# Performance work log

Measured on AMD Instinct MI355X. Metric: run time of the kernel, lower is better.

Reference implementation:

```python
import jax, jax.numpy as jnp
import numpy as np

B, T, S0 = 8, 4, 4096
D_MODEL, H, D, R, RANK = 2048, 16, 128, 64, 512
C = D - R  # content dim = 64


def _rope(x, positions):
    # x: [B, H, T, R]; rotate-half style RoPE as in the torch module
    half = x.shape[-1] // 2
    inv_freq = 1.0 / (10000.0 ** (jnp.arange(half, dtype=jnp.float32) / half))
    freqs = positions.astype(jnp.float32)[:, None] * inv_freq[None, :]  # [T, half]
    cos = jnp.cos(freqs)[None, None].astype(x.dtype)
    sin = jnp.sin(freqs)[None, None].astype(x.dtype)
    x1, x2 = x[..., :half], x[..., half:]
    return jnp.concatenate([x1 * cos - x2 * sin, x1 * sin + x2 * cos], axis=-1)


def setup_inputs() -> dict:
    key = jax.random.key(0)
    ks = jax.random.split(key, 9)
    s = 0.02
    return {
        "x": jax.random.normal(ks[0], (B, T, D_MODEL), jnp.float32),
        "cache_c_kv": jax.random.normal(ks[1], (B, S0, RANK), jnp.float32),
        "cache_k_rope": jax.random.normal(ks[2], (B, S0, H, R), jnp.float32),
        "w_q": jax.random.normal(ks[3], (D_MODEL, H * C), jnp.float32) * s,
        "w_q_rope": jax.random.normal(ks[4], (D_MODEL, H * R), jnp.float32) * s,
        "w_kv_down": jax.random.normal(ks[5], (D_MODEL, RANK), jnp.float32) * s,
        "w_kv_up": jax.random.normal(ks[6], (RANK, H * D), jnp.float32) * s,
        "w_k_rope": jax.random.normal(ks[7], (D_MODEL, H * R), jnp.float32) * s,
        "w_out": jax.random.normal(ks[8], (H * D, D_MODEL), jnp.float32) * s,
    }


def reference(x, cache_c_kv, cache_k_rope, w_q, w_q_rope, w_kv_down, w_kv_up, w_k_rope, w_out):
    cache_len = cache_c_kv.shape[1]
    positions = jnp.arange(cache_len, cache_len + T)

    # queries
    q_content = (x @ w_q).reshape(B, T, H, C).transpose(0, 2, 1, 3)        # [B,H,T,C]
    q_rope = (x @ w_q_rope).reshape(B, T, H, R).transpose(0, 2, 1, 3)      # [B,H,T,R]
    q_rope = _rope(q_rope, positions)
    q = jnp.concatenate([q_content, q_rope], axis=-1)                       # [B,H,T,D]

    # new compressed kv + rope keys, append to cache
    c_kv_new = x @ w_kv_down                                                # [B,T,RANK]
    k_rope_new = (x @ w_k_rope).reshape(B, T, H, R).transpose(0, 2, 1, 3)
    k_rope_new = _rope(k_rope_new, positions).transpose(0, 2, 1, 3)         # [B,T,H,R]
    c_kv = jnp.concatenate([cache_c_kv, c_kv_new], axis=1)                  # [B,S,RANK]
    k_rope = jnp.concatenate([cache_k_rope, k_rope_new], axis=1)            # [B,S,H,R]

    # decompress full cache every step (the expensive MLA pattern)
    S = c_kv.shape[1]
    kv = (c_kv @ w_kv_up).reshape(B, S, H, D)                               # [B,S,H,D]
    k_content = kv[..., :C].transpose(0, 2, 1, 3)                           # [B,H,S,C]
    v = kv.transpose(0, 2, 1, 3)                                            # [B,H,S,D]
    k = jnp.concatenate([k_content, k_rope.transpose(0, 2, 1, 3)], axis=-1) # [B,H,S,D]

    # kv_cache present => is_prefill False => no causal mask (faithful to source)
    scale = 1.0 / jnp.sqrt(jnp.asarray(D, dtype=q.dtype))
    scores = jnp.einsum('bhtd,bhsd->bhts', q, k) * scale
    attn = jax.nn.softmax(scores, axis=-1)
    out = jnp.einsum('bhts,bhsd->bhtd', attn, v)                            # [B,H,T,D]
    out = out.transpose(0, 2, 1, 3).reshape(B, T, H * D)
    return out @ w_out                                                       # [B,T,D_MODEL]
```

## Files before the change

kernel.cpp:

```cpp
#include <hip/hip_runtime.h>
#include <hip/hip_fp16.h>
#include <cmath>

#define BB 8
#define TT 4
#define HH 16
#define DDIM 128
#define RRDIM 64
#define CCDIM 64
#define RANKC 512
#define DMODEL 2048
#define S0C 4096
#define NQ 64
#define HD 2048
#define NACT 3584
#define NSC 65
#define NG 17
#define SPAD 4160
#define SCALE_ATT 0.08838834764831845f

typedef __attribute__((ext_vector_type(8))) short bf16x8;
typedef __attribute__((ext_vector_type(4))) float f32x4;
typedef unsigned short ushortT;

#define AIDX(row, kk) ((row)*132 + (((row)>>2)<<2) + (kk))

static __device__ __forceinline__ unsigned short f2bf(float x) {
  unsigned u = __float_as_uint(x);
  u += 0x7FFFu + ((u >> 16) & 1u);
  return (unsigned short)(u >> 16);
}
static __device__ __forceinline__ unsigned pk2(float a, float b) {
  return (unsigned)f2bf(a) | ((unsigned)f2bf(b) << 16);
}

__global__ __launch_bounds__(256) void k_front(const float* __restrict__ A,
                                               const float* __restrict__ w0,
                                               const float* __restrict__ w1,
                                               const float* __restrict__ w2,
                                               const float* __restrict__ w3,
                                               const float* __restrict__ cckv,
                                               float* __restrict__ part,
                                               ushortT* __restrict__ ckvB,
                                               ushortT* __restrict__ ckvT,
                                               float* __restrict__ rctab) {
  __shared__ float shf[4352];
  const int tid = threadIdx.x;
  const int bx = blockIdx.x;
  if (bx < 448) {
    const int cb = bx % 28;
    const int k0 = (bx / 28) * 128;
    const float* W; int N, lc0, off;
    if (cb < 8)       { W = w0; N = 1024; lc0 = cb * 128;        off = 0; }
    else if (cb < 16) { W = w1; N = 1024; lc0 = (cb - 8) * 128;  off = 1024; }
    else if (cb < 20) { W = w2; N = 512;  lc0 = (cb - 16) * 128; off = 2048; }
    else              { W = w3; N = 1024; lc0 = (cb - 20) * 128; off = 2560; }
    {
      const int row = tid >> 3;
      const int kseg = (tid & 7) * 16;
      const float4* s4 = reinterpret_cast<const float4*>(A + (size_t)row * DMODEL + k0 + kseg);
      float4 v0 = s4[0], v1 = s4[1], v2 = s4[2], v3 = s4[3];
      *reinterpret_cast<float4*>(&shf[AIDX(row, kseg)])      = v0;
      *reinterpret_cast<float4*>(&shf[AIDX(row, kseg + 4)])  = v1;
      *reinterpret_cast<float4*>(&shf[AIDX(row, kseg + 8)])  = v2;
      *reinterpret_cast<float4*>(&shf[AIDX(row, kseg + 12)]) = v3;
    }
    __syncthreads();
    const int cg = tid & 31;
    const int rg = tid >> 5;
    float acc[4][4];
    #pragma unroll
    for (int r = 0; r < 4; ++r)
      #pragma unroll
      for (int c = 0; c < 4; ++c) acc[r][c] = 0.f;
    #pragma unroll 4
    for (int kk = 0; kk < 128; ++kk) {
      const float4 w4 = *reinterpret_cast<const float4*>(W + (size_t)(k0 + kk) * N + lc0 + cg * 4);
      const float wv[4] = {w4.x, w4.y, w4.z, w4.w};
      #pragma unroll
      for (int r = 0; r < 4; ++r) {
        const float av = shf[AIDX(rg * 4 + r, kk)];
        #pragma unroll
        for (int c = 0; c < 4; ++c) acc[r][c] = fmaf(av, wv[c], acc[r][c]);
      }
    }
    #pragma unroll
    for (int r = 0; r < 4; ++r) {
      float4 o = make_float4(acc[r][0], acc[r][1], acc[r][2], acc[r][3]);
      *reinterpret_cast<float4*>(part + ((size_t)(bx / 28) * 32 + rg * 4 + r) * NACT + off + lc0 + cg * 4) = o;
    }
  } else if (bx < 960) {
    ushortT* tlds = reinterpret_cast<ushortT*>(shf);
    const int idx = bx - 448;
    const int b = idx >> 6, c = idx & 63;
    const float* src = cckv + ((size_t)b * S0C + c * 64) * RANKC;
    ushortT* dstB = ckvB + ((size_t)(b * NSC + c) * 64) * RANKC;
    ushortT* dstT = ckvT + ((size_t)(b * NSC + c) * RANKC) * 64;
    const int s = tid >> 2, rq = tid & 3;
    const int rloc = tid >> 1, shalf = (tid & 1) * 32;
    for (int slab = 0; slab < 4; ++slab) {
      const int r0 = slab * 128;
      unsigned pk_arr[16];
      #pragma unroll
      for (int i = 0; i < 8; ++i) {
        const float4 v = *reinterpret_cast<const float4*>(src + (size_t)s * RANKC + r0 + rq * 32 + i * 4);
        pk_arr[2 * i]     = pk2(v.x, v.y);
        pk_arr[2 * i + 1] = pk2(v.z, v.w);
        *reinterpret_cast<uint2*>(&tlds[s * 136 + rq * 32 + i * 4]) =
            make_uint2(pk_arr[2 * i], pk_arr[2 * i + 1]);
      }
      {
        uint4* db = reinterpret_cast<uint4*>(dstB + (size_t)s * RANKC + r0 + rq * 32);
        db[0] = make_uint4(pk_arr[0], pk_arr[1], pk_arr[2], pk_arr[3]);
        db[1] = make_uint4(pk_arr[4], pk_arr[5], pk_arr[6], pk_arr[7]);
        db[2] = make_uint4(pk_arr[8], pk_arr[9], pk_arr[10], pk_arr[11]);
        db[3] = make_uint4(pk_arr[12], pk_arr[13], pk_arr[14], pk_arr[15]);
      }
      __syncthreads();
      unsigned pkv[16];
      #pragma unroll
      for (int k = 0; k < 16; ++k) {
        const unsigned t0 = tlds[(shalf + 2 * k)     * 136 + rloc];
        const unsigned t1 = tlds[(shalf + 2 * k + 1) * 136 + rloc];
        pkv[k] = t0 | (t1 << 16);
      }
      uint4* d = reinterpret_cast<uint4*>(dstT + ((size_t)(r0 + rloc)) * 64 + shalf);
      d[0] = make_uint4(pkv[0], pkv[1], pkv[2], pkv[3]);
      d[1] = make_uint4(pkv[4], pkv[5], pkv[6], pkv[7]);
      d[2] = make_uint4(pkv[8], pkv[9], pkv[10], pkv[11]);
      d[3] = make_uint4(pkv[12], pkv[13], pkv[14], pkv[15]);
      __syncthreads();
    }
  } else {
    const int b = bx - 960;
    const uint4 z = make_uint4(0, 0, 0, 0);
    uint4* p = reinterpret_cast<uint4*>(ckvT + ((size_t)(b * NSC + 64) * RANKC) * 64);
    for (int i = tid; i < 4096; i += 256) p[i] = z;
    uint4* q = reinterpret_cast<uint4*>(ckvB + (((size_t)(b * NSC + 64) * 64) + 4) * RANKC);
    for (int i = tid; i < 3840; i += 256) q[i] = z;
    if (bx == 960 && tid < 128) {
      const int t = tid >> 5, j = tid & 31;
      const double fr = (double)(S0C + t) * pow(10000.0, -(double)j / 32.0);
      rctab[t * 32 + j]       = (float)cos(fr);
      rctab[128 + t * 32 + j] = (float)sin(fr);
    }
  }
}

__global__ __launch_bounds__(256) void k_mid(const float* __restrict__ part0,
                                             const float* __restrict__ cache_kr,
                                             const float* __restrict__ wup,
                                             const float* __restrict__ rctab,
                                             ushortT* __restrict__ qlat,
                                             ushortT* __restrict__ ckvB,
                                             ushortT* __restrict__ ckvT,
                                             __half* __restrict__ rs) {
  __shared__ float smid[2176];
  const int tid = threadIdx.x;
  const int bx = blockIdx.x;
  if (bx < 1152) {
    const int bh = bx / 9, sy = bx % 9;
    const int b = bh >> 4, h = bh & 15;
    float* raw_q = smid;
    float* raw_k = smid + 256;
    float* qr_l  = smid + 512;
    float* kr_l  = smid + 768;
    {
      const int t = tid >> 6, j = tid & 63;
      const size_t rowoff = (size_t)(b * TT + t) * NACT;
      float sq = 0.f, sk = 0.f;
      #pragma unroll 4
      for (int ks = 0; ks < 16; ++ks) {
        const float* pp = part0 + (size_t)ks * (32 * NACT) + rowoff;
        sq += pp[1024 + h * 64 + j];
        sk += pp[2560 + h * 64 + j];
      }
      raw_q[t * 64 + j] = sq;
      raw_k[t * 64 + j] = sk;
    }
    __syncthreads();
    {
      const int t = tid >> 6, j = tid & 63;
      const int j2 = j & 31;
      const float cs = rctab[t * 32 + j2];
      const float sn = rctab[128 + t * 32 + j2];
      const float qa = raw_q[t * 64 + j], qp = raw_q[t * 64 + (j ^ 32)];
      const float ka = raw_k[t * 64 + j], kp = raw_k[t * 64 + (j ^ 32)];
      float qv, kv;
      if (j < 32) { qv = qa * cs - qp * sn; kv = ka * cs - kp * sn; }
      else        { qv = qp * sn + qa * cs; kv = kp * sn + ka * cs; }
      qr_l[t * 64 + j] = qv * SCALE_ATT;
      kr_l[t * 64 + j] = kv;
    }
    __syncthreads();
    const int ql = tid & 3;
    float4 qf[4][4];
    #pragma unroll
    for (int t = 0; t < 4; ++t)
      #pragma unroll
      for (int u = 0; u < 4; ++u)
        qf[t][u] = *reinterpret_cast<const float4*>(&qr_l[t * 64 + ql * 16 + u * 4]);
    const int s0 = sy * 512;
    #pragma unroll 2
    for (int pass = 0; pass < 8; ++pass) {
      const int s = s0 + pass * 64 + (tid >> 2);
      if (s < 4100) {
        float p[4] = {0.f, 0.f, 0.f, 0.f};
        const float* krow = (s < S0C)
            ? cache_kr + (((size_t)b * S0C + s) * HH + h) * RRDIM
            : &kr_l[(s - S0C) * 64];
        #pragma unroll
        for (int u = 0; u < 4; ++u) {
          const float4 kv = *reinterpret_cast<const float4*>(krow + ql * 16 + u * 4);
          #pragma unroll
          for (int t = 0; t < 4; ++t)
            p[t] += kv.x * qf[t][u].x + kv.y * qf[t][u].y
                  + kv.z * qf[t][u].z + kv.w * qf[t][u].w;
        }
        #pragma unroll
        for (int t = 0; t < 4; ++t) {
          p[t] += __shfl_xor(p[t], 1, 4);
          p[t] += __shfl_xor(p[t], 2, 4);
        }
        rs[((size_t)bh * 4 + ql) * SPAD + s] = __float2half(p[ql]);
      }
    }
  } else if (bx < 1216) {
    const int lx = bx - 1152;
    const int h = lx & 15;
    const int r0 = (lx >> 4) * 128;
    float* a_s = smid;
    {
      const int bt = tid >> 3;
      const int c8 = (tid & 7) * 8;
      float v[8] = {0.f,0.f,0.f,0.f,0.f,0.f,0.f,0.f};
      #pragma unroll 4
      for (int ks = 0; ks < 16; ++ks) {
        const float4* pp = reinterpret_cast<const float4*>(
            part0 + (size_t)ks * (32 * NACT) + (size_t)bt * NACT + h * CCDIM + c8);
        const float4 x0 = pp[0], x1 = pp[1];
        v[0]+=x0.x; v[1]+=x0.y; v[2]+=x0.z; v[3]+=x0.w;
        v[4]+=x1.x; v[5]+=x1.y; v[6]+=x1.z; v[7]+=x1.w;
      }
      #pragma unroll
      for (int u = 0; u < 8; ++u) a_s[bt * 68 + c8 + u] = v[u];
    }
    __syncthreads();
    const int r = tid & 127;
    const int bth = tid >> 7;
    const float* wrow = wup + (size_t)(r0 + r) * HD + h * DDIM;
    float4 wreg[16];
    #pragma unroll
    for (int u = 0; u < 16; ++u)
      wreg[u] = *reinterpret_cast<const float4*>(wrow + u * 4);
    float acc[16];
    #pragma unroll
    for (int i = 0; i < 16; ++i) acc[i] = 0.f;
    #pragma unroll
    for (int u = 0; u < 16; ++u) {
      #pragma unroll
      for (int i = 0; i < 16; ++i) {
        const float4 av = *reinterpret_cast<const float4*>(&a_s[(bth * 16 + i) * 68 + u * 4]);
        acc[i] = fmaf(av.x, wreg[u].x, acc[i]);
        acc[i] = fmaf(av.y, wreg[u].y, acc[i]);
        acc[i] = fmaf(av.z, wreg[u].z, acc[i]);
        acc[i] = fmaf(av.w, wreg[u].w, acc[i]);
      }
    }
    #pragma unroll
    for (int i = 0; i < 16; ++i) {
      const int bt = bth * 16 + i;
      const int b = bt >> 2, t = bt & 3;
      qlat[((size_t)(b * NQ) + h * TT + t) * RANKC + r0 + r] = f2bf(acc[i]);
    }
  } else {
    const int g = (bx - 1216) * 256 + tid;
    const int r = g & 511;
    const int bt = g >> 9;
    const int b = bt >> 2, t = bt & 3;
    float s = 0.f;
    #pragma unroll 4
    for (int ks = 0; ks < 16; ++ks)
      s += part0[(size_t)ks * (32 * NACT) + (size_t)bt * NACT + 2048 + r];
    const ushortT bv = f2bf(s);
    ckvB[(((size_t)(b * NSC + 64) * 64) + t) * RANKC + r] = bv;
    ckvT[(((size_t)(b * NSC + 64) * RANKC) + r) * 64 + t] = bv;
  }
}

__global__ __launch_bounds__(256) void k_att(
    const ushortT* __restrict__ ckvB, const ushortT* __restrict__ ckvT,
    const ushortT* __restrict__ qlat, const __half* __restrict__ rs,
    float* __restrict__ olat, float* __restrict__ mlg) {
  __shared__ ushortT PL[4][32 * 72];
  __shared__ float mlS[4][2][32];
  __shared__ float wS[4][32];
  const int tid = threadIdx.x;
  const int wv = tid >> 6;
  const int lane = tid & 63;
  const int lm = lane & 15, lg = lane >> 4;
  const int g = blockIdx.x, b = blockIdx.y, qh = blockIdx.z;
  const int qbase = qh * 32;
  const int nc = (g < 16) ? 4 : 1;
  const int c0 = (g < 16) ? g * 4 : 64;

  if (wv < nc) {
    const int myc = c0 + wv;
    const int scnt = (myc < 64) ? 64 : TT;
    const ushortT* bsrc = ckvB + ((size_t)(b * NSC + myc) * 64) * RANKC;
    const ushortT* qrow = qlat + ((size_t)b * NQ + qbase + lm) * RANKC + lg * 8;
    f32x4 acc[2][4];
    #pragma unroll
    for (int qm = 0; qm < 2; ++qm)
      #pragma unroll
      for (int st = 0; st < 4; ++st) acc[qm][st] = (f32x4){0.f, 0.f, 0.f, 0.f};
    #pragma unroll
    for (int ks = 0; ks < 16; ++ks) {
      const bf16x8 qa0 = *reinterpret_cast<const bf16x8*>(qrow + ks * 32);
      const bf16x8 qa1 = *reinterpret_cast<const bf16x8*>(qrow + 16 * RANKC + ks * 32);
      #pragma unroll
      for (int st = 0; st < 4; ++st) {
        const bf16x8 bf = *reinterpret_cast<const bf16x8*>(
            bsrc + (size_t)(st * 16 + lm) * RANKC + ks * 32 + lg * 8);
        acc[0][st] = __builtin_amdgcn_mfma_f32_16x16x32_bf16(qa0, bf, acc[0][st], 0, 0, 0);
        acc[1][st] = __builtin_amdgcn_mfma_f32_16x16x32_bf16(qa1, bf, acc[1][st], 0, 0, 0);
      }
    }
    #pragma unroll
    for (int qm = 0; qm < 2; ++qm) {
      #pragma unroll
      for (int reg = 0; reg < 4; ++reg) {
        const int ql = qm * 16 + lg * 4 + reg;
        const int qi = qbase + ql;
        const __half* rp = rs + (((size_t)(b * HH) + (qi >> 2)) * TT + (qi & 3)) * SPAD + myc * 64;
        float vvv[4];
        float mx = -1e30f;
        #pragma unroll
        for (int st = 0; st < 4; ++st) {
          const int sl = st * 16 + lm;
          const float val = (sl < scnt)
              ? fmaf(acc[qm][st][reg], SCALE_ATT, __half2float(rp[sl]))
              : -1e30f;
          vvv[st] = val;
          mx = fmaxf(mx, val);
        }
        #pragma unroll
        for (int off = 1; off < 16; off <<= 1) mx = fmaxf(mx, __shfl_xor(mx, off, 16));
        float sum = 0.f;
        #pragma unroll
        for (int st = 0; st < 4; ++st) {
          const float p = __expf(vvv[st] - mx);
          vvv[st] = p;
          sum += p;
        }
        #pragma unroll
        for (int off = 1; off < 16; off <<= 1) sum += __shfl_xor(sum, off, 16);
        #pragma unroll
        for (int st = 0; st < 4; ++st)
          PL[wv][ql * 72 + st * 16 + lm] = f2bf(vvv[st]);
        if (lm == 0) { mlS[wv][0][ql] = mx; mlS[wv][1][ql] = sum; }
      }
    }
  }
  __syncthreads();

  if (tid < 32) {
    const int q = tid;
    float mg = -1e30f;
    for (int c = 0; c < nc; ++c) mg = fmaxf(mg, mlS[c][0][q]);
    float la = 0.f;
    for (int c = 0; c < nc; ++c) {
      const float w = __expf(mlS[c][0][q] - mg);
      wS[c][q] = w;
      la = fmaf(mlS[c][1][q], w, la);
    }
    const size_t gb = (((size_t)b * NG + g) * NQ + qbase + q) * 2;
    mlg[gb] = mg; mlg[gb + 1] = la;
  }
  __syncthreads();

  const int rg = wv;
  f32x4 OACC[2][8];
  #pragma unroll
  for (int qm = 0; qm < 2; ++qm)
    #pragma unroll
    for (int rn = 0; rn < 8; ++rn) OACC[qm][rn] = (f32x4){0.f, 0.f, 0.f, 0.f};
  for (int c = 0; c < nc; ++c) {
    const bf16x8 pa00 = *reinterpret_cast<const bf16x8*>(&PL[c][lm * 72 + lg * 8]);
    const bf16x8 pa01 = *reinterpret_cast<const bf16x8*>(&PL[c][lm * 72 + 32 + lg * 8]);
    const bf16x8 pa10 = *reinterpret_cast<const bf16x8*>(&PL[c][(16 + lm) * 72 + lg * 8]);
    const bf16x8 pa11 = *reinterpret_cast<const bf16x8*>(&PL[c][(16 + lm) * 72 + 32 + lg * 8]);
    const f32x4 w0 = {wS[c][lg * 4 + 0], wS[c][lg * 4 + 1], wS[c][lg * 4 + 2], wS[c][lg * 4 + 3]};
    const f32x4 w1 = {wS[c][16 + lg * 4 + 0], wS[c][16 + lg * 4 + 1],
                      wS[c][16 + lg * 4 + 2], wS[c][16 + lg * 4 + 3]};
    const ushortT* vb = ckvT + ((size_t)(b * NSC + c0 + c) * RANKC + rg * 128 + lm) * 64 + lg * 8;
    #pragma unroll
    for (int rn = 0; rn < 8; ++rn) {
      const bf16x8 b0 = *reinterpret_cast<const bf16x8*>(vb + (size_t)rn * 16 * 64);
      const bf16x8 b1 = *reinterpret_cast<const bf16x8*>(vb + (size_t)rn * 16 * 64 + 32);
      f32x4 t0 = (f32x4){0.f, 0.f, 0.f, 0.f}, t1 = (f32x4){0.f, 0.f, 0.f, 0.f};
      t0 = __builtin_amdgcn_mfma_f32_16x16x32_bf16(pa00, b0, t0, 0, 0, 0);
      t0 = __builtin_amdgcn_mfma_f32_16x16x32_bf16(pa01, b1, t0, 0, 0, 0);
      t1 = __builtin_amdgcn_mfma_f32_16x16x32_bf16(pa10, b0, t1, 0, 0, 0);
      t1 = __builtin_amdgcn_mfma_f32_16x16x32_bf16(pa11, b1, t1, 0, 0, 0);
      OACC[0][rn] += w0 * t0;
      OACC[1][rn] += w1 * t1;
    }
  }
  const size_t obase = ((size_t)(b * NG + g) * NQ) * RANKC;
  #pragma unroll
  for (int qm = 0; qm < 2; ++qm)
    #pragma unroll
    for (int rn = 0; rn < 8; ++rn)
      #pragma unroll
      for (int reg = 0; reg < 4; ++reg)
        olat[obase + (size_t)(qbase + qm * 16 + lg * 4 + reg) * RANKC + rg * 128 + rn * 16 + lm]
            = OACC[qm][rn][reg];
}

__global__ __launch_bounds__(512) void k_combF(const float* __restrict__ mlg,
                                               const float* __restrict__ olat,
                                               const float* __restrict__ wup,
                                               float* __restrict__ ohead,
                                               float* __restrict__ out) {
  __shared__ float wrow[4][20];
  __shared__ float att_lds[4][516];
  __shared__ float red[4][4][32][4];
  const int h = blockIdx.x, b = blockIdx.y;
  const int tid = threadIdx.x;
  {
    const int t = tid >> 7, col = tid & 127;
    out[(size_t)(b * TT + t) * HD + h * DDIM + col] = 0.f;
  }
  const int wave = tid >> 6;
  const int i = wave >> 1;
  const int rhalf = wave & 1;
  const int rl = tid & 63;
  const int qi = h * TT + i;
  float m1 = -1e30f, l1 = 0.f;
  if (rl < NG) {
    const size_t base = (((size_t)b * NG + rl) * NQ + qi) * 2;
    m1 = mlg[base]; l1 = mlg[base + 1];
  }
  float M = m1;
  #pragma unroll
  for (int off = 1; off < 64; off <<= 1) M = fmaxf(M, __shfl_xor(M, off));
  float L = (rl < NG) ? l1 * __expf(m1 - M) : 0.f;
  #pragma unroll
  for (int off = 1; off < 64; off <<= 1) L += __shfl_xor(L, off);
  const float invL = 1.0f / L;
  if (rl < NG) wrow[i][rl] = __expf(m1 - M) * invL;
  __syncthreads();
  const int r0 = rhalf * 256 + rl * 4;
  {
    float o0 = 0.f, o1 = 0.f, o2 = 0.f, o3 = 0.f;
    for (int c = 0; c < NG; ++c) {
      const float w = wrow[i][c];
      const float4 v = *reinterpret_cast<const float4*>(
          olat + (((size_t)b * NG + c) * NQ + qi) * RANKC + r0);
      o0 = fmaf(v.x, w, o0); o1 = fmaf(v.y, w, o1);
      o2 = fmaf(v.z, w, o2); o3 = fmaf(v.w, w, o3);
    }
    *reinterpret_cast<float4*>(&att_lds[i][r0]) = make_float4(o0, o1, o2, o3);
  }
  __syncthreads();
  const int t = tid >> 7;
  const int rq = (tid >> 5) & 3;
  const int c4 = tid & 31;
  const float* wb = wup + (size_t)h * DDIM + c4 * 4;
  float a0 = 0.f, a1 = 0.f, a2 = 0.f, a3 = 0.f;
  const int rbeg = rq * 128;
  #pragma unroll 4
  for (int rr = 0; rr < 128; ++rr) {
    const int r = rbeg + rr;
    const float4 w4 = *reinterpret_cast<const float4*>(wb + (size_t)r * HD);
    const float a = att_lds[t][r];
    a0 = fmaf(a, w4.x, a0); a1 = fmaf(a, w4.y, a1);
    a2 = fmaf(a, w4.z, a2); a3 = fmaf(a, w4.w, a3);
  }
  *reinterpret_cast<float4*>(&red[rq][t][c4][0]) = make_float4(a0, a1, a2, a3);
  __syncthreads();
  if (tid < 128) {
    const int t2 = tid >> 5, c42 = tid & 31;
    float4 s = make_float4(0.f, 0.f, 0.f, 0.f);
    #pragma unroll
    for (int q = 0; q < 4; ++q) {
      const float4 v = *reinterpret_cast<const float4*>(&red[q][t2][c42][0]);
      s.x += v.x; s.y += v.y; s.z += v.z; s.w += v.w;
    }
    *reinterpret_cast<float4*>(&ohead[(size_t)(b * TT + t2) * HD + h * DDIM + c42 * 4]) = s;
  }
}

__global__ __launch_bounds__(256) void k_projA(const float* __restrict__ A,
                                               const float* __restrict__ W,
                                               float* __restrict__ out) {
  __shared__ float a_lds[4352];
  const int tid = threadIdx.x;
  const int c0 = blockIdx.x * 128;
  const int k0 = blockIdx.y * 128;
  {
    const int row = tid >> 3;
    const int kseg = (tid & 7) * 16;
    const float4* s4 = reinterpret_cast<const float4*>(A + (size_t)row * DMODEL + k0 + kseg);
    float4 v0 = s4[0], v1 = s4[1], v2 = s4[2], v3 = s4[3];
    *reinterpret_cast<float4*>(&a_lds[AIDX(row, kseg)])      = v0;
    *reinterpret_cast<float4*>(&a_lds[AIDX(row, kseg + 4)])  = v1;
    *reinterpret_cast<float4*>(&a_lds[AIDX(row, kseg + 8)])  = v2;
    *reinterpret_cast<float4*>(&a_lds[AIDX(row, kseg + 12)]) = v3;
  }
  __syncthreads();
  const int cg = tid & 31;
  const int rg = tid >> 5;
  float acc[4][4];
  #pragma unroll
  for (int r = 0; r < 4; ++r)
    #pragma unroll
    for (int c = 0; c < 4; ++c) acc[r][c] = 0.f;
  #pragma unroll 4
  for (int kk = 0; kk < 128; ++kk) {
    const float4 w4 = *reinterpret_cast<const float4*>(W + (size_t)(k0 + kk) * HD + c0 + cg * 4);
    const float wv[4] = {w4.x, w4.y, w4.z, w4.w};
    #pragma unroll
    for (int r = 0; r < 4; ++r) {
      const float av = a_lds[AIDX(rg * 4 + r, kk)];
      #pragma unroll
      for (int c = 0; c < 4; ++c) acc[r][c] = fmaf(av, wv[c], acc[r][c]);
    }
  }
  #pragma unroll
  for (int r = 0; r < 4; ++r)
    #pragma unroll
    for (int c = 0; c < 4; ++c)
      unsafeAtomicAdd(&out[(size_t)(rg * 4 + r) * HD + c0 + cg * 4 + c], acc[r][c]);
}

extern "C" void kernel_launch(void* const* d_in, const int* in_sizes, int n_in,
                              void* d_out, int out_size, void* d_ws, size_t ws_size,
                              hipStream_t stream) {
  const float* x     = (const float*)d_in[0];
  const float* cckv  = (const float*)d_in[1];
  const float* ckr   = (const float*)d_in[2];
  const float* w_q   = (const float*)d_in[3];
  const float* w_qr  = (const float*)d_in[4];
  const float* w_kvd = (const float*)d_in[5];
  const float* w_kvu = (const float*)d_in[6];
  const float* w_kr  = (const float*)d_in[7];
  const float* w_out = (const float*)d_in[8];
  float* out = (float*)d_out;
  float* ws = (float*)d_ws;

  size_t off = 0;
  ushortT* qlat   = (ushortT*)(ws + off); off += 131072;
  float* mlgb     = ws + off; off += (size_t)BB * NG * NQ * 2;
  float* ohead    = ws + off; off += 65536;
  float* rctab    = ws + off; off += 256;
  __half* rsb     = (__half*)(ws + off); off += 1064960;
  ushortT* ckvB   = (ushortT*)(ws + off); off += 8519680;
  ushortT* ckvT   = (ushortT*)(ws + off); off += 8519680;
  float* regB  = ws + off;
  float* part0 = regB;
  float* olat  = regB;

  k_front<<<dim3(968), 256, 0, stream>>>(x, w_q, w_qr, w_kvd, w_kr, cckv, part0, ckvB, ckvT, rctab);
  k_mid<<<dim3(1280), 256, 0, stream>>>(part0, ckr, w_kvu, rctab, qlat, ckvB, ckvT, rsb);
  k_att<<<dim3(NG, BB, 2), 256, 0, stream>>>(ckvB, ckvT, qlat, rsb, olat, mlgb);
  k_combF<<<dim3(16, 8), 512, 0, stream>>>(mlgb, olat, w_kvu, ohead, out);
  k_projA<<<dim3(16, 16), 256, 0, stream>>>(ohead, w_out, out);
}
```

Baseline: 194.6 us.

## Fold rope scores into attention MFMA via block-diagonal bf16 key layout

```diff
diff --git a/kernel.cpp b/kernel.cpp
--- a/kernel.cpp
+++ b/kernel.cpp
@@ -1,5 +1,4 @@
 #include <hip/hip_runtime.h>
-#include <hip/hip_fp16.h>
 #include <cmath>
 
 #define BB 8
@@ -16,7 +15,9 @@
 #define NACT 3584
 #define NSC 65
 #define NG 17
-#define SPAD 4160
+#define KX 1536
+#define KRW 1024
+#define NKR 4160
 #define SCALE_ATT 0.08838834764831845f
 
 typedef __attribute__((ext_vector_type(8))) short bf16x8;
@@ -40,9 +41,12 @@
                                                const float* __restrict__ w2,
                                                const float* __restrict__ w3,
                                                const float* __restrict__ cckv,
+                                               const float* __restrict__ ckr,
                                                float* __restrict__ part,
                                                ushortT* __restrict__ ckvB,
                                                ushortT* __restrict__ ckvT,
+                                               ushortT* __restrict__ krB,
+                                               ushortT* __restrict__ qlatX,
                                                float* __restrict__ rctab) {
   __shared__ float shf[4352];
   const int tid = threadIdx.x;
@@ -131,14 +135,36 @@
       d[3] = make_uint4(pkv[12], pkv[13], pkv[14], pkv[15]);
       __syncthreads();
     }
+  } else if (bx < 3008) {
+    const int idx = bx - 960;
+    const int b = idx >> 8, rblk = idx & 255;
+    const int row = rblk * 16 + (tid >> 4);
+    const int cseg = (tid & 15) * 64;
+    const float* src = ckr + ((size_t)(b * S0C) + row) * KRW + cseg;
+    ushortT* dst = krB + ((size_t)(b * NKR) + row) * KRW + cseg;
+    unsigned pk_arr[32];
+    #pragma unroll
+    for (int i = 0; i < 16; ++i) {
+      const float4 v = *reinterpret_cast<const float4*>(src + i * 4);
+      pk_arr[2 * i]     = pk2(v.x, v.y);
+      pk_arr[2 * i + 1] = pk2(v.z, v.w);
+    }
+    uint4* d = reinterpret_cast<uint4*>(dst);
+    #pragma unroll
+    for (int i = 0; i < 8; ++i)
+      d[i] = make_uint4(pk_arr[4 * i], pk_arr[4 * i + 1], pk_arr[4 * i + 2], pk_arr[4 * i + 3]);
   } else {
-    const int b = bx - 960;
+    const int b = bx - 3008;
     const uint4 z = make_uint4(0, 0, 0, 0);
     uint4* p = reinterpret_cast<uint4*>(ckvT + ((size_t)(b * NSC + 64) * RANKC) * 64);
     for (int i = tid; i < 4096; i += 256) p[i] = z;
     uint4* q = reinterpret_cast<uint4*>(ckvB + (((size_t)(b * NSC + 64) * 64) + 4) * RANKC);
     for (int i = tid; i < 3840; i += 256) q[i] = z;
-    if (bx == 960 && tid < 128) {
+    uint4* k4 = reinterpret_cast<uint4*>(krB + ((size_t)(b * NKR) + 4100) * KRW);
+    for (int i = tid; i < 7680; i += 256) k4[i] = z;
+    uint4* qx = reinterpret_cast<uint4*>(qlatX + (size_t)b * NQ * KX);
+    for (int i = tid; i < 12288; i += 256) qx[i] = z;
+    if (bx == 3008 && tid < 128) {
       const int t = tid >> 5, j = tid & 31;
       const double fr = (double)(S0C + t) * pow(10000.0, -(double)j / 32.0);
       rctab[t * 32 + j]       = (float)cos(fr);
@@ -148,87 +174,18 @@
 }
 
 __global__ __launch_bounds__(256) void k_mid(const float* __restrict__ part0,
-                                             const float* __restrict__ cache_kr,
                                              const float* __restrict__ wup,
                                              const float* __restrict__ rctab,
-                                             ushortT* __restrict__ qlat,
+                                             ushortT* __restrict__ qlatX,
                                              ushortT* __restrict__ ckvB,
                                              ushortT* __restrict__ ckvT,
-                                             __half* __restrict__ rs) {
-  __shared__ float smid[2176];
+                                             ushortT* __restrict__ krB) {
+  __shared__ float smid[8192];
   const int tid = threadIdx.x;
   const int bx = blockIdx.x;
-  if (bx < 1152) {
-    const int bh = bx / 9, sy = bx % 9;
-    const int b = bh >> 4, h = bh & 15;
-    float* raw_q = smid;
-    float* raw_k = smid + 256;
-    float* qr_l  = smid + 512;
-    float* kr_l  = smid + 768;
-    {
-      const int t = tid >> 6, j = tid & 63;
-      const size_t rowoff = (size_t)(b * TT + t) * NACT;
-      float sq = 0.f, sk = 0.f;
-      #pragma unroll 4
-      for (int ks = 0; ks < 16; ++ks) {
-        const float* pp = part0 + (size_t)ks * (32 * NACT) + rowoff;
-        sq += pp[1024 + h * 64 + j];
-        sk += pp[2560 + h * 64 + j];
-      }
-      raw_q[t * 64 + j] = sq;
-      raw_k[t * 64 + j] = sk;
-    }
-    __syncthreads();
-    {
-      const int t = tid >> 6, j = tid & 63;
-      const int j2 = j & 31;
-      const float cs = rctab[t * 32 + j2];
-      const float sn = rctab[128 + t * 32 + j2];
-      const float qa = raw_q[t * 64 + j], qp = raw_q[t * 64 + (j ^ 32)];
-      const float ka = raw_k[t * 64 + j], kp = raw_k[t * 64 + (j ^ 32)];
-      float qv, kv;
-      if (j < 32) { qv = qa * cs - qp * sn; kv = ka * cs - kp * sn; }
-      else        { qv = qp * sn + qa * cs; kv = kp * sn + ka * cs; }
-      qr_l[t * 64 + j] = qv * SCALE_ATT;
-      kr_l[t * 64 + j] = kv;
-    }
-    __syncthreads();
-    const int ql = tid & 3;
-    float4 qf[4][4];
-    #pragma unroll
-    for (int t = 0; t < 4; ++t)
-      #pragma unroll
-      for (int u = 0; u < 4; ++u)
-        qf[t][u] = *reinterpret_cast<const float4*>(&qr_l[t * 64 + ql * 16 + u * 4]);
-    const int s0 = sy * 512;
-    #pragma unroll 2
-    for (int pass = 0; pass < 8; ++pass) {
-      const int s = s0 + pass * 64 + (tid >> 2);
-      if (s < 4100) {
-        float p[4] = {0.f, 0.f, 0.f, 0.f};
-        const float* krow = (s < S0C)
-            ? cache_kr + (((size_t)b * S0C + s) * HH + h) * RRDIM
-            : &kr_l[(s - S0C) * 64];
-        #pragma unroll
-        for (int u = 0; u < 4; ++u) {
-          const float4 kv = *reinterpret_cast<const float4*>(krow + ql * 16 + u * 4);
-          #pragma unroll
-          for (int t = 0; t < 4; ++t)
-            p[t] += kv.x * qf[t][u].x + kv.y * qf[t][u].y
-                  + kv.z * qf[t][u].z + kv.w * qf[t][u].w;
-        }
-        #pragma unroll
-        for (int t = 0; t < 4; ++t) {
-          p[t] += __shfl_xor(p[t], 1, 4);
-          p[t] += __shfl_xor(p[t], 2, 4);
-        }
-        rs[((size_t)bh * 4 + ql) * SPAD + s] = __float2half(p[ql]);
-      }
-    }
-  } else if (bx < 1216) {
-    const int lx = bx - 1152;
-    const int h = lx & 15;
-    const int r0 = (lx >> 4) * 128;
+  if (bx < 64) {
+    const int h = bx & 15;
+    const int r0 = (bx >> 4) * 128;
     float* a_s = smid;
     {
       const int bt = tid >> 3;
@@ -271,10 +228,42 @@
     for (int i = 0; i < 16; ++i) {
       const int bt = bth * 16 + i;
       const int b = bt >> 2, t = bt & 3;
-      qlat[((size_t)(b * NQ) + h * TT + t) * RANKC + r0 + r] = f2bf(acc[i]);
+      qlatX[((size_t)(b * NQ) + h * TT + t) * KX + r0 + r] = f2bf(acc[i]);
+    }
+  } else if (bx < 72) {
+    const int b = bx - 64;
+    float* rawq = smid;
+    float* rawk = smid + 4096;
+    #pragma unroll
+    for (int r = 0; r < 16; ++r) {
+      const int idx = r * 256 + tid;
+      const int h = idx >> 8, t = (idx >> 6) & 3, j = idx & 63;
+      float sq = 0.f, sk = 0.f;
+      #pragma unroll 4
+      for (int ks = 0; ks < 16; ++ks) {
+        const float* base = part0 + (size_t)ks * (32 * NACT) + (size_t)(b * TT + t) * NACT;
+        sq += base[1024 + h * 64 + j];
+        sk += base[2560 + h * 64 + j];
+      }
+      rawq[idx] = sq;
+      rawk[idx] = sk;
+    }
+    __syncthreads();
+    #pragma unroll
+    for (int r = 0; r < 16; ++r) {
+      const int idx = r * 256 + tid;
+      const int h = idx >> 8, t = (idx >> 6) & 3, j = idx & 63, j2 = j & 31;
+      const float cs = rctab[t * 32 + j2];
+      const float sn = rctab[128 + t * 32 + j2];
+      const float qa = rawq[idx], qp = rawq[idx ^ 32];
+      const float ka = rawk[idx], kp = rawk[idx ^ 32];
+      const float qv = (j < 32) ? (qa * cs - qp * sn) : (qp * sn + qa * cs);
+      const float kv = (j < 32) ? (ka * cs - kp * sn) : (kp * sn + ka * cs);
+      qlatX[((size_t)(b * NQ) + h * TT + t) * KX + 512 + h * 64 + j] = f2bf(qv);
+      krB[((size_t)(b * NKR) + S0C + t) * KRW + h * 64 + j] = f2bf(kv);
     }
   } else {
-    const int g = (bx - 1216) * 256 + tid;
+    const int g = (bx - 72) * 256 + tid;
     const int r = g & 511;
     const int bt = g >> 9;
     const int b = bt >> 2, t = bt & 3;
@@ -290,7 +279,7 @@
 
 __global__ __launch_bounds__(256) void k_att(
     const ushortT* __restrict__ ckvB, const ushortT* __restrict__ ckvT,
-    const ushortT* __restrict__ qlat, const __half* __restrict__ rs,
+    const ushortT* __restrict__ krB, const ushortT* __restrict__ qlatX,
     float* __restrict__ olat, float* __restrict__ mlg) {
   __shared__ ushortT PL[4][32 * 72];
   __shared__ float mlS[4][2][32];
@@ -308,7 +297,8 @@
     const int myc = c0 + wv;
     const int scnt = (myc < 64) ? 64 : TT;
     const ushortT* bsrc = ckvB + ((size_t)(b * NSC + myc) * 64) * RANKC;
-    const ushortT* qrow = qlat + ((size_t)b * NQ + qbase + lm) * RANKC + lg * 8;
+    const ushortT* ksrc = krB + ((size_t)(b * NKR) + myc * 64) * KRW;
+    const ushortT* qrow = qlatX + ((size_t)b * NQ + qbase + lm) * KX + lg * 8;
     f32x4 acc[2][4];
     #pragma unroll
     for (int qm = 0; qm < 2; ++qm)
@@ -317,7 +307,7 @@
     #pragma unroll
     for (int ks = 0; ks < 16; ++ks) {
       const bf16x8 qa0 = *reinterpret_cast<const bf16x8*>(qrow + ks * 32);
-      const bf16x8 qa1 = *reinterpret_cast<const bf16x8*>(qrow + 16 * RANKC + ks * 32);
+      const bf16x8 qa1 = *reinterpret_cast<const bf16x8*>(qrow + 16 * KX + ks * 32);
       #pragma unroll
       for (int st = 0; st < 4; ++st) {
         const bf16x8 bf = *reinterpret_cast<const bf16x8*>(
@@ -326,21 +316,29 @@
         acc[1][st] = __builtin_amdgcn_mfma_f32_16x16x32_bf16(qa1, bf, acc[1][st], 0, 0, 0);
       }
     }
+    #pragma unroll 8
+    for (int kx = 0; kx < 32; ++kx) {
+      const bf16x8 qa0 = *reinterpret_cast<const bf16x8*>(qrow + 512 + kx * 32);
+      const bf16x8 qa1 = *reinterpret_cast<const bf16x8*>(qrow + 16 * KX + 512 + kx * 32);
+      #pragma unroll
+      for (int st = 0; st < 4; ++st) {
+        const bf16x8 bf = *reinterpret_cast<const bf16x8*>(
+            ksrc + (size_t)(st * 16 + lm) * KRW + kx * 32 + lg * 8);
+        acc[0][st] = __builtin_amdgcn_mfma_f32_16x16x32_bf16(qa0, bf, acc[0][st], 0, 0, 0);
+        acc[1][st] = __builtin_amdgcn_mfma_f32_16x16x32_bf16(qa1, bf, acc[1][st], 0, 0, 0);
+      }
+    }
     #pragma unroll
     for (int qm = 0; qm < 2; ++qm) {
       #pragma unroll
       for (int reg = 0; reg < 4; ++reg) {
         const int ql = qm * 16 + lg * 4 + reg;
-        const int qi = qbase + ql;
-        const __half* rp = rs + (((size_t)(b * HH) + (qi >> 2)) * TT + (qi & 3)) * SPAD + myc * 64;
         float vvv[4];
         float mx = -1e30f;
         #pragma unroll
         for (int st = 0; st < 4; ++st) {
           const int sl = st * 16 + lm;
-          const float val = (sl < scnt)
-              ? fmaf(acc[qm][st][reg], SCALE_ATT, __half2float(rp[sl]))
-              : -1e30f;
+          const float val = (sl < scnt) ? acc[qm][st][reg] * SCALE_ATT : -1e30f;
           vvv[st] = val;
           mx = fmaxf(mx, val);
         }
@@ -551,20 +549,21 @@
   float* ws = (float*)d_ws;
 
   size_t off = 0;
-  ushortT* qlat   = (ushortT*)(ws + off); off += 131072;
+  ushortT* qlatX  = (ushortT*)(ws + off); off += 393216;
   float* mlgb     = ws + off; off += (size_t)BB * NG * NQ * 2;
   float* ohead    = ws + off; off += 65536;
   float* rctab    = ws + off; off += 256;
-  __half* rsb     = (__half*)(ws + off); off += 1064960;
   ushortT* ckvB   = (ushortT*)(ws + off); off += 8519680;
   ushortT* ckvT   = (ushortT*)(ws + off); off += 8519680;
+  ushortT* krB    = (ushortT*)(ws + off); off += 17039360;
   float* regB  = ws + off;
   float* part0 = regB;
   float* olat  = regB;
 
-  k_front<<<dim3(968), 256, 0, stream>>>(x, w_q, w_qr, w_kvd, w_kr, cckv, part0, ckvB, ckvT, rctab);
-  k_mid<<<dim3(1280), 256, 0, stream>>>(part0, ckr, w_kvu, rctab, qlat, ckvB, ckvT, rsb);
-  k_att<<<dim3(NG, BB, 2), 256, 0, stream>>>(ckvB, ckvT, qlat, rsb, olat, mlgb);
+  k_front<<<dim3(3016), 256, 0, stream>>>(x, w_q, w_qr, w_kvd, w_kr, cckv, ckr,
+                                          part0, ckvB, ckvT, krB, qlatX, rctab);
+  k_mid<<<dim3(136), 256, 0, stream>>>(part0, w_kvu, rctab, qlatX, ckvB, ckvT, krB);
+  k_att<<<dim3(NG, BB, 2), 256, 0, stream>>>(ckvB, ckvT, krB, qlatX, olat, mlgb);
   k_combF<<<dim3(16, 8), 512, 0, stream>>>(mlgb, olat, w_kvu, ohead, out);
   k_projA<<<dim3(16, 16), 256, 0, stream>>>(ohead, w_out, out);
 }
```

Result: slower. 281.7 us (+44.7%).
